# Optimization experiments

Measured on AMD Instinct MI355X. Metric: run time of the kernel, lower is better.

Reference implementation:

```python
import jax, jax.numpy as jnp
import numpy as np
import math

B, S, D, H, HD, M, E = 4, 1024, 1024, 16, 64, 4096, 1024
EPS = 1e-6

def rms_norm(x, w):
    # torch: x / (||x||/sqrt(d) + eps) * w  (eps added to the norm, not norm^2)
    n = jnp.sqrt(jnp.sum(x * x, axis=-1, keepdims=True)) / math.sqrt(x.shape[-1])
    return x / (n + EPS) * w

def rope(x):
    # x: (B,H,S,hd)
    hd, s = x.shape[-1], x.shape[2]
    inv = 1.0 / (10000.0 ** (jnp.arange(0, hd, 2, dtype=jnp.float32) / hd))
    fr = jnp.arange(s, dtype=jnp.float32)[:, None] * inv[None, :]        # (S, hd/2)
    emb = jnp.concatenate([fr, fr], axis=-1)                              # (S, hd)
    cos, sin = jnp.cos(emb), jnp.sin(emb)
    x1, x2 = x[..., : hd // 2], x[..., hd // 2 :]
    rot = jnp.concatenate([-x2, x1], axis=-1)
    return x * cos + rot * sin

def setup_inputs() -> dict:
    key = jax.random.key(0)
    ks = jax.random.split(key, 18)
    p = lambda k, sh: jax.random.normal(k, sh, jnp.float32) * 0.02
    return {
        'x': jax.random.normal(ks[0], (B, S, D), jnp.float32),
        'emb': jax.random.normal(ks[1], (B, E), jnp.float32),
        'ln1_w': jnp.ones((D,), jnp.float32),
        'ln1_lW': p(ks[2], (E, 2 * D)), 'ln1_lb': p(ks[3], (2 * D,)),
        'ln2_w': jnp.ones((D,), jnp.float32),
        'ln2_lW': p(ks[4], (E, 2 * D)), 'ln2_lb': p(ks[5], (2 * D,)),
        'qkv_W': p(ks[6], (D, 3 * D)), 'qkv_b': p(ks[7], (3 * D,)),
        'proj_W': p(ks[8], (D, D)), 'proj_b': p(ks[9], (D,)),
        'nq_w': jnp.ones((HD,), jnp.float32), 'nk_w': jnp.ones((HD,), jnp.float32),
        'mlp_W': p(ks[10], (D, 2 * M)), 'mlp_b': p(ks[11], (2 * M,)),
        'out_W': p(ks[12], (M, D)), 'out_b': p(ks[13], (D,)),
        'gates_W': p(ks[14], (E, 2 * D)), 'gates_b': p(ks[15], (2 * D,)),
    }

def reference(x, emb, ln1_w, ln1_lW, ln1_lb, ln2_w, ln2_lW, ln2_lb,
              qkv_W, qkv_b, proj_W, proj_b, nq_w, nk_w,
              mlp_W, mlp_b, out_W, out_b, gates_W, gates_b):
    g = emb @ gates_W + gates_b                       # (B, 2D)
    gate_mha, gate_mlp = g[:, :D], g[:, D:]
    # AdaLNZero 1
    ss = emb @ ln1_lW + ln1_lb                        # (B, 2D): [scale | shift]
    xn = rms_norm(x, ln1_w) * (1.0 + ss[:, None, :D]) + ss[:, None, D:]
    # RoPE attention with qk RMSNorm
    qkv = (xn @ qkv_W + qkv_b).reshape(B, S, 3, H, HD).transpose(2, 0, 3, 1, 4)
    q, k, v = qkv[0], qkv[1], qkv[2]                  # each (B,H,S,HD)
    q = rms_norm(rope(q), nq_w)
    k = rms_norm(rope(k), nk_w)
    scores = jnp.einsum('bhqd,bhkd->bhqk', q, k) * (HD ** -0.5)
    attn = jnp.nan_to_num(jax.nn.softmax(scores, axis=-1))
    ao = jnp.einsum('bhqk,bhkd->bhqd', attn, v).transpose(0, 2, 1, 3).reshape(B, S, D)
    x = x + gate_mha[:, None, :] * (ao @ proj_W + proj_b)
    # AdaLNZero 2 + SwiGLU MLP
    ss2 = emb @ ln2_lW + ln2_lb
    xn2 = rms_norm(x, ln2_w) * (1.0 + ss2[:, None, :D]) + ss2[:, None, D:]
    h = xn2 @ mlp_W + mlp_b                           # (B,S,2M)
    act = h[..., :M] * jax.nn.silu(h[..., M:])
    mlp_out = act @ out_W + out_b
    return x + gate_mlp[:, None, :] * mlp_out
```

## Files before the change

kernel.cpp:

```cpp
#include <hip/hip_runtime.h>
#include <hip/hip_bf16.h>
#include <math.h>

#define B_ 4
#define S_ 1024
#define D_ 1024
#define H_ 16
#define HD_ 64
#define M_ 4096
#define E_ 1024

using bf16 = __hip_bfloat16;
typedef short bf16x8 __attribute__((ext_vector_type(8)));
typedef float f32x4 __attribute__((ext_vector_type(4)));

__device__ __forceinline__ void gl_lds16(const void* g, void* l) {
    __builtin_amdgcn_global_load_lds(
        (__attribute__((address_space(1))) void*)(g),
        (__attribute__((address_space(3))) void*)(l), 16, 0, 0);
}



#define STG_A(q, pb, kc) gl_lds16(A  + gAoff[q] + (kc), &sA[pb][(q) * 4096 + tid * 8])
#define STG_B(q, pb, kc) gl_lds16(Bt + gBoff[q] + (kc), &sB[pb][(q) * 4096 + tid * 8])

#define LDA(mh, m, h) (*(const bf16x8*)(cA + aRow + (mh) * 8192 + (m) * 2048 + (h)))
#define LDB(nh, n, h) (*(const bf16x8*)(cB + bRow + (nh) * 4096 + (n) * 2048 + (h)))

#define MFMA_QUAD(MH, NH, BF)                                                             \
    __builtin_amdgcn_s_setprio(1);                                                        \
    _Pragma("unroll")                                                                     \
    for (int m = 0; m < 4; ++m) {                                                         \
        _Pragma("unroll")                                                                 \
        for (int n = 0; n < 2; ++n) {                                                     \
            acc[(MH)*4+m][(NH)*2+n] = __builtin_amdgcn_mfma_f32_16x16x32_bf16(            \
                aF[m][0], BF[n][0], acc[(MH)*4+m][(NH)*2+n], 0, 0, 0);                    \
            acc[(MH)*4+m][(NH)*2+n] = __builtin_amdgcn_mfma_f32_16x16x32_bf16(            \
                aF[m][1], BF[n][1], acc[(MH)*4+m][(NH)*2+n], 0, 0, 0);                    \
        }                                                                                 \
    }                                                                                     \
    __builtin_amdgcn_s_setprio(0);

#define GEMM256_LOOP                                                                      \
    const int nt = K >> 6;                                                                \
    for (int t = 0; t < nt; ++t) {                                                        \
        const int pb = t & 1;                                                             \
        const char* cA = (const char*)sA[pb];                                             \
        const char* cB = (const char*)sB[pb];                                             \
        const int kc2 = (t + 2) << 6;                                                     \
        const bool pf = (t + 2) < nt;                                                     \
        bf16x8 aF[4][2], b0F[2][2], b1F[2][2];                                            \
                                          \
        _Pragma("unroll")                                                                 \
        for (int m = 0; m < 4; ++m) {                                                     \
            aF[m][0] = LDA(0, m, cs0);                                                    \
            aF[m][1] = LDA(0, m, cs1);                                                    \
        }                                                                                 \
        _Pragma("unroll")                                                                 \
        for (int n = 0; n < 2; ++n) {                                                     \
            b0F[n][0] = LDB(0, n, cs0);                                                   \
            b0F[n][1] = LDB(0, n, cs1);                                                   \
        }                                                                                 \
        __builtin_amdgcn_s_barrier();                                                     \
        asm volatile("s_waitcnt lgkmcnt(0)" ::: "memory");                                \
        MFMA_QUAD(0, 0, b0F)                                                              \
        __builtin_amdgcn_s_barrier();                                                     \
                         \
        _Pragma("unroll")                                                                 \
        for (int n = 0; n < 2; ++n) {                                                     \
            b1F[n][0] = LDB(1, n, cs0);                                                   \
            b1F[n][1] = LDB(1, n, cs1);                                                   \
        }                                                                                 \
        if (pf) { STG_A(0, pb, kc2); STG_A(2, pb, kc2); }                                 \
        __builtin_amdgcn_s_barrier();                                                     \
        asm volatile("s_waitcnt lgkmcnt(0)" ::: "memory");                                \
        MFMA_QUAD(0, 1, b1F)                                                              \
        __builtin_amdgcn_s_barrier();                                                     \
                               \
        _Pragma("unroll")                                                                 \
        for (int m = 0; m < 4; ++m) {                                                     \
            aF[m][0] = LDA(1, m, cs0);                                                    \
            aF[m][1] = LDA(1, m, cs1);                                                    \
        }                                                                                 \
        if (pf) { STG_B(0, pb, kc2); STG_B(1, pb, kc2);                                   \
                  STG_B(2, pb, kc2); STG_B(3, pb, kc2); }                                 \
        __builtin_amdgcn_s_barrier();                                                     \
        asm volatile("s_waitcnt lgkmcnt(0)" ::: "memory");                                \
        MFMA_QUAD(1, 1, b1F)                                                              \
        __builtin_amdgcn_s_barrier();                                                     \
                                 \
        if (pf) { STG_A(1, pb, kc2); STG_A(3, pb, kc2); }                                 \
        __builtin_amdgcn_s_barrier();                                                     \
        asm volatile("s_waitcnt lgkmcnt(0)" ::: "memory");                                \
        MFMA_QUAD(1, 0, b0F)                                                              \
        if (pf)              { asm volatile("s_waitcnt vmcnt(8)" ::: "memory"); }         \
        else if (t + 1 < nt) { asm volatile("s_waitcnt vmcnt(0)" ::: "memory"); }         \
        __builtin_amdgcn_s_barrier();                                                     \
    }

#define GEMM256_PROLOG(NPN, N0MUL)                                                        \
    const int tid = threadIdx.x;                                                          \
    const int wave = tid >> 6, lane = tid & 63;                                           \
    const int wr = wave >> 2, wc = wave & 3;                                              \
    const int cl = lane & 15, qd = lane >> 4;                                             \
    const int num_pid_n = (NPN);                                                          \
    const int cpx = gridDim.x >> 3;                                                       \
    int wg = (blockIdx.x & 7) * cpx + (blockIdx.x >> 3);                                  \
    const int group_size = 8 * num_pid_n;                                                 \
    const int group_id = wg / group_size;                                                 \
    const int pid_in = wg - group_id * group_size;                                        \
    const int m0 = (group_id * 8 + (pid_in & 7)) * 256;                                   \
    const int n0 = (pid_in >> 3) * (N0MUL);

__global__ __launch_bounds__(256) void ropetab_kernel(float4* __restrict__ tab)
{
    int idx = blockIdx.x * 256 + threadIdx.x;
    int s = idx >> 4, j = idx & 15;
    float inv0 = exp2f(-(float)j        * (13.287712379549449f / 32.f));
    float inv1 = exp2f(-(float)(16 + j) * (13.287712379549449f / 32.f));
    float sn0, c0, sn1, c1;
    sincosf((float)s * inv0, &sn0, &c0);
    sincosf((float)s * inv1, &sn1, &c1);
    tab[idx] = make_float4(c0, sn0, c1, sn1);
}

__global__ __launch_bounds__(256) void transpose_all_kernel(
    const float* __restrict__ W0, bf16* __restrict__ T0,
    const float* __restrict__ W1, bf16* __restrict__ T1,
    const float* __restrict__ W2, bf16* __restrict__ T2,
    const float* __restrict__ W3, bf16* __restrict__ T3)
{
    __shared__ float tile[32][33];
    int id = blockIdx.x;
    const float* W; bf16* T; int K, N, bx, by;
    if (id < 3072)       { W = W0; T = T0; K = 1024; N = 3072; bx = id % 96;  by = id / 96; }
    else if (id < 4096)  { id -= 3072;  W = W1; T = T1; K = 1024; N = 1024; bx = id & 31;  by = id >> 5; }
    else if (id < 12288) { id -= 4096;  W = W2; T = T2; K = 1024; N = 8192; bx = id & 255; by = id >> 8; }
    else                 { id -= 12288; W = W3; T = T3; K = 4096; N = 1024; bx = id & 31;  by = id >> 5; }
    int n0 = bx * 32, k0 = by * 32;
    int tx = threadIdx.x & 31, ty = threadIdx.x >> 5;
    #pragma unroll
    for (int r = ty; r < 32; r += 8)
        tile[r][tx] = W[(long)(k0 + r) * N + n0 + tx];
    __syncthreads();
    #pragma unroll
    for (int r = ty; r < 32; r += 8)
        T[(long)(n0 + r) * K + k0 + tx] = __float2bfloat16(tile[tx][r]);
}

__global__ __launch_bounds__(256) void embgemm_kernel(
    const float* __restrict__ emb,
    const float* __restrict__ W0, const float* __restrict__ b0,
    const float* __restrict__ W1, const float* __restrict__ b1,
    const float* __restrict__ W2, const float* __restrict__ b2,
    float* __restrict__ G, float* __restrict__ SS, float* __restrict__ SS2)
{
    __shared__ float se[256];
    int b = blockIdx.y;
    int k0 = blockIdx.z * 256;
    if (threadIdx.x < 256) se[threadIdx.x] = emb[b * 1024 + k0 + threadIdx.x];
    __syncthreads();
    int j = blockIdx.x * 256 + threadIdx.x;
    int which = j >> 11, col = j & 2047;
    const float* W  = which == 0 ? W0 : (which == 1 ? W1 : W2);
    const float* bb = which == 0 ? b0 : (which == 1 ? b1 : b2);
    float acc = (k0 == 0) ? bb[col] : 0.f;
    #pragma unroll 4
    for (int k = 0; k < 256; ++k) acc += se[k] * W[(long)(k0 + k) * 2048 + col];
    float* out = which == 0 ? G : (which == 1 ? SS : SS2);
    atomicAdd(&out[b * 2048 + col], acc);
}

__global__ __launch_bounds__(256) void rmsmod_kernel(
    const float* __restrict__ x, const float* __restrict__ w,
    const float* __restrict__ ss, bf16* __restrict__ out)
{
    int row = blockIdx.x;
    int b = row >> 10;
    const float* xr = x + (long)row * D_;
    float4 v = ((const float4*)xr)[threadIdx.x];
    float ssum = v.x * v.x + v.y * v.y + v.z * v.z + v.w * v.w;
    #pragma unroll
    for (int off = 32; off; off >>= 1) ssum += __shfl_xor(ssum, off);
    __shared__ float red[4];
    if ((threadIdx.x & 63) == 0) red[threadIdx.x >> 6] = ssum;
    __syncthreads();
    float tot = red[0] + red[1] + red[2] + red[3];
    float n = sqrtf(tot) * (1.f / 32.f);
    float inv = 1.f / (n + 1e-6f);
    int d0 = threadIdx.x * 4;
    const float* ssb = ss + b * 2048;
    bf16 t[4];
    t[0] = __float2bfloat16(v.x * inv * w[d0 + 0] * (1.f + ssb[d0 + 0]) + ssb[D_ + d0 + 0]);
    t[1] = __float2bfloat16(v.y * inv * w[d0 + 1] * (1.f + ssb[d0 + 1]) + ssb[D_ + d0 + 1]);
    t[2] = __float2bfloat16(v.z * inv * w[d0 + 2] * (1.f + ssb[d0 + 2]) + ssb[D_ + d0 + 2]);
    t[3] = __float2bfloat16(v.w * inv * w[d0 + 3] * (1.f + ssb[d0 + 3]) + ssb[D_ + d0 + 3]);
    *(uint2*)&out[(long)row * D_ + d0] = *(uint2*)t;
}

__global__ __launch_bounds__(512) void qkvgemm_kernel(
    const bf16* __restrict__ A, const bf16* __restrict__ Bt,
    const float* __restrict__ bias,
    const float* __restrict__ nq_w, const float* __restrict__ nk_w,
    const float4* __restrict__ ropetab,
    bf16* __restrict__ qh, bf16* __restrict__ kh, bf16* __restrict__ vt,
    int N, int K)
{
    __shared__ bf16 sA[2][16384];
    __shared__ bf16 sB[2][16384];
    GEMM256_PROLOG(N >> 8, 256)

    long gAoff[4], gBoff[4];
    #pragma unroll
    for (int q = 0; q < 4; ++q) {
        int c = tid + q * 512;
        int cs = c ^ ((c >> 3) & 7);
        int row = cs >> 3, col = (cs & 7) * 8;
        gAoff[q] = (long)(m0 + row) * K + col;
        gBoff[q] = (long)(n0 + row) * K + col;
    }

    #pragma unroll
    for (int q = 0; q < 4; ++q) { STG_A(q, 0, 0); STG_B(q, 0, 0); }
    #pragma unroll
    for (int q = 0; q < 4; ++q) { STG_A(q, 1, 64); STG_B(q, 1, 64); }

    f32x4 acc[8][4] = {};
    const int swz = (cl & 7) << 4;
    const int aRow = (wr * 128 + cl) * 128;
    const int bRow = (wc * 64 + cl) * 128;
    const int cs0 = (qd * 16) ^ swz;
    const int cs1 = (qd * 16 + 64) ^ swz;

    asm volatile("s_waitcnt vmcnt(8)" ::: "memory");
    __builtin_amdgcn_s_barrier();

    GEMM256_LOOP

    const int third = n0 >> 10;
    const int h = ((n0 & 1023) >> 6) + wc;
    const int b = m0 >> 10;
    const int s0 = (m0 & 1023) + wr * 128;
    const int colb = n0 + wc * 64;
    float bs0 = bias[colb + cl],      bs1 = bias[colb + 16 + cl];
    float bs2 = bias[colb + 32 + cl], bs3 = bias[colb + 48 + cl];

    if (third == 2) {
        #pragma unroll
        for (int n = 0; n < 4; ++n) {
            int d = n * 16 + cl;
            float bs = bias[colb + n * 16 + cl];
            long rowd = ((long)(b * 16 + h) * 64 + d) * 1024;
            #pragma unroll
            for (int m = 0; m < 8; ++m) {
                int sb = s0 + m * 16 + qd * 4;
                bf16 t4[4];
                #pragma unroll
                for (int i = 0; i < 4; ++i)
                    t4[i] = __float2bfloat16(acc[m][n][i] + bs);
                *(uint2*)&vt[rowd + sb] = *(uint2*)t4;
            }
        }
    } else {
        const float* w = (third == 0) ? nq_w : nk_w;
        bf16* dst = (third == 0) ? qh : kh;
        float w0 = w[cl], w1 = w[16 + cl], w2 = w[32 + cl], w3 = w[48 + cl];
        long hb = ((long)(b * 16 + h) * 1024) * 64;
        #pragma unroll
        for (int m = 0; m < 8; ++m) {
            #pragma unroll
            for (int i = 0; i < 4; ++i) {
                int s = s0 + m * 16 + qd * 4 + i;
                float v0 = acc[m][0][i] + bs0, v1 = acc[m][1][i] + bs1;
                float v2 = acc[m][2][i] + bs2, v3 = acc[m][3][i] + bs3;
                float4 cs = ropetab[s * 16 + cl];
                float r0 = v0 * cs.x - v2 * cs.y;
                float r1 = v1 * cs.z - v3 * cs.w;
                float r2 = v2 * cs.x + v0 * cs.y;
                float r3 = v3 * cs.z + v1 * cs.w;
                float ssq = r0 * r0 + r1 * r1 + r2 * r2 + r3 * r3;
                ssq += __shfl_xor(ssq, 1);
                ssq += __shfl_xor(ssq, 2);
                ssq += __shfl_xor(ssq, 4);
                ssq += __shfl_xor(ssq, 8);
                float innv = 1.f / (sqrtf(ssq) * 0.125f + 1e-6f);
                long ro = hb + (long)s * 64;
                dst[ro + cl]      = __float2bfloat16(r0 * innv * w0);
                dst[ro + 16 + cl] = __float2bfloat16(r1 * innv * w1);
                dst[ro + 32 + cl] = __float2bfloat16(r2 * innv * w2);
                dst[ro + 48 + cl] = __float2bfloat16(r3 * innv * w3);
            }
        }
    }
}

__global__ __launch_bounds__(512) void gemm256_mlp_kernel(
    const bf16* __restrict__ A, const bf16* __restrict__ Bt,
    const float* __restrict__ bias, bf16* __restrict__ ACT, int K)
{
    __shared__ bf16 sA[2][16384];
    __shared__ bf16 sB[2][16384];
    GEMM256_PROLOG(32, 128)

    long gAoff[4], gBoff[4];
    #pragma unroll
    for (int q = 0; q < 4; ++q) {
        int c = tid + q * 512;
        int cs = c ^ ((c >> 3) & 7);
        int row = cs >> 3, col = (cs & 7) * 8;
        gAoff[q] = (long)(m0 + row) * K + col;
        int pp = row >> 5, hf = (row >> 4) & 1, wi = row & 15;
        gBoff[q] = (long)(hf * 4096 + n0 + pp * 16 + wi) * K + col;
    }

    #pragma unroll
    for (int q = 0; q < 4; ++q) { STG_A(q, 0, 0); STG_B(q, 0, 0); }
    #pragma unroll
    for (int q = 0; q < 4; ++q) { STG_A(q, 1, 64); STG_B(q, 1, 64); }

    f32x4 acc[8][4] = {};
    const int swz = (cl & 7) << 4;
    const int aRow = (wr * 128 + cl) * 128;
    const int bRow = (wc * 64 + cl) * 128;
    const int cs0 = (qd * 16) ^ swz;
    const int cs1 = (qd * 16 + 64) ^ swz;

    asm volatile("s_waitcnt vmcnt(8)" ::: "memory");
    __builtin_amdgcn_s_barrier();

    GEMM256_LOOP

    #pragma unroll
    for (int m = 0; m < 8; ++m) {
        #pragma unroll
        for (int pr = 0; pr < 2; ++pr) {
            int col = n0 + wc * 32 + pr * 16 + cl;
            float bs1 = bias[col];
            float bs2 = bias[4096 + col];
            #pragma unroll
            for (int i = 0; i < 4; ++i) {
                int row = m0 + wr * 128 + m * 16 + qd * 4 + i;
                float h1 = acc[m][pr * 2 + 0][i] + bs1;
                float h2 = acc[m][pr * 2 + 1][i] + bs2;
                float sg = 1.f / (1.f + __expf(-h2));
                ACT[(long)row * 4096 + col] = __float2bfloat16(h1 * h2 * sg);
            }
        }
    }
}

#define MFMA_HQ(MH)                                                                       \
    __builtin_amdgcn_s_setprio(1);                                                        \
    _Pragma("unroll")                                                                     \
    for (int m = 0; m < 4; ++m) {                                                         \
        _Pragma("unroll")                                                                 \
        for (int n = 0; n < 2; ++n) {                                                     \
            acc[(MH)*4+m][n] = __builtin_amdgcn_mfma_f32_16x16x32_bf16(                   \
                aF[m][0], bF[n][0], acc[(MH)*4+m][n], 0, 0, 0);                           \
            acc[(MH)*4+m][n] = __builtin_amdgcn_mfma_f32_16x16x32_bf16(                   \
                aF[m][1], bF[n][1], acc[(MH)*4+m][n], 0, 0, 0);                           \
        }                                                                                 \
    }                                                                                     \
    __builtin_amdgcn_s_setprio(0);

__global__ __launch_bounds__(512) void gemm256x128_kernel(
    const bf16* __restrict__ A, const bf16* __restrict__ Bt,
    float* __restrict__ P0, float* __restrict__ P1, int N, int K)
{
    __shared__ bf16 sA[2][16384];
    __shared__ bf16 sB[2][8192];
    const int tid = threadIdx.x;
    const int wave = tid >> 6, lane = tid & 63;
    const int wr = wave >> 2, wc = wave & 3;
    const int cl = lane & 15, qd = lane >> 4;

    const int cpx = gridDim.x >> 3;
    int wg = (blockIdx.x & 7) * cpx + (blockIdx.x >> 3);
    const int split = wg >> 7;
    const int w2 = wg & 127;
    const int group_id = w2 >> 6;
    const int pid_in = w2 & 63;
    const int m0 = (group_id * 8 + (pid_in & 7)) * 256;
    const int n0 = (pid_in >> 3) * 128;
    const int Kh = K >> 1;
    A  += (long)split * Kh;
    Bt += (long)split * Kh;

    long gAoff[4], gBoff[2];
    #pragma unroll
    for (int q = 0; q < 4; ++q) {
        int c = tid + q * 512;
        int cs = c ^ ((c >> 3) & 7);
        int row = cs >> 3, col = (cs & 7) * 8;
        gAoff[q] = (long)(m0 + row) * K + col;
        if (q < 2) gBoff[q] = (long)(n0 + row) * K + col;
    }

    const int nt = Kh >> 6;
    STG_A(0, 0, 0); STG_A(2, 0, 0); STG_B(0, 0, 0); STG_B(1, 0, 0);
    STG_A(1, 0, 0); STG_A(3, 0, 0);
    if (nt > 1) { STG_A(0, 1, 64); STG_A(2, 1, 64); STG_B(0, 1, 64); STG_B(1, 1, 64); }

    f32x4 acc[8][2] = {};
    const int swz = (cl & 7) << 4;
    const int aRow = (wr * 128 + cl) * 128;
    const int bRow = (wc * 32 + cl) * 128;
    const int cs0 = (qd * 16) ^ swz;
    const int cs1 = (qd * 16 + 64) ^ swz;

    if (nt > 1) { asm volatile("s_waitcnt vmcnt(4)" ::: "memory"); }
    else        { asm volatile("s_waitcnt vmcnt(0)" ::: "memory"); }
    __builtin_amdgcn_s_barrier();

    for (int t = 0; t < nt; ++t) {
        const int pb = t & 1;
        const char* cA = (const char*)sA[pb];
        const char* cB = (const char*)sB[pb];
        bf16x8 aF[4][2], bF[2][2];
        #pragma unroll
        for (int m = 0; m < 4; ++m) {
            aF[m][0] = *(const bf16x8*)(cA + aRow + m * 2048 + cs0);
            aF[m][1] = *(const bf16x8*)(cA + aRow + m * 2048 + cs1);
        }
        #pragma unroll
        for (int n = 0; n < 2; ++n) {
            bF[n][0] = *(const bf16x8*)(cB + bRow + n * 2048 + cs0);
            bF[n][1] = *(const bf16x8*)(cB + bRow + n * 2048 + cs1);
        }
        if (t + 1 < nt) { STG_A(1, pb ^ 1, (t + 1) << 6); STG_A(3, pb ^ 1, (t + 1) << 6); }
        __builtin_amdgcn_s_barrier();
        asm volatile("s_waitcnt lgkmcnt(0)" ::: "memory");
        MFMA_HQ(0)
        __builtin_amdgcn_s_barrier();
        #pragma unroll
        for (int m = 0; m < 4; ++m) {
            aF[m][0] = *(const bf16x8*)(cA + aRow + 8192 + m * 2048 + cs0);
            aF[m][1] = *(const bf16x8*)(cA + aRow + 8192 + m * 2048 + cs1);
        }
        if (t + 2 < nt) { STG_A(0, pb, (t + 2) << 6); STG_A(2, pb, (t + 2) << 6);
                          STG_B(0, pb, (t + 2) << 6); STG_B(1, pb, (t + 2) << 6); }
        __builtin_amdgcn_s_barrier();
        asm volatile("s_waitcnt lgkmcnt(0)" ::: "memory");
        MFMA_HQ(1)
        if (t + 2 < nt)      { asm volatile("s_waitcnt vmcnt(4)" ::: "memory"); }
        else if (t + 1 < nt) { asm volatile("s_waitcnt vmcnt(0)" ::: "memory"); }
        __builtin_amdgcn_s_barrier();
    }

    float* P = split ? P1 : P0;
    #pragma unroll
    for (int m = 0; m < 8; ++m) {
        #pragma unroll
        for (int n = 0; n < 2; ++n) {
            int col = n0 + wc * 32 + n * 16 + cl;
            #pragma unroll
            for (int i = 0; i < 4; ++i) {
                int row = m0 + wr * 128 + m * 16 + qd * 4 + i;
                P[(long)row * N + col] = acc[m][n][i];
            }
        }
    }
}

__global__ __launch_bounds__(256) void fuseout_kernel(
    const float* __restrict__ p0, const float* __restrict__ p1,
    const float* __restrict__ bias, const float* __restrict__ resid,
    const float* __restrict__ gates, float* __restrict__ out)
{
    int idx = blockIdx.x * 256 + threadIdx.x;
    int row = idx >> 8;
    int b = row >> 10;
    int c4 = (idx & 255) * 4;
    float4 a = ((const float4*)p0)[idx];
    float4 c = ((const float4*)p1)[idx];
    float4 r = ((const float4*)resid)[idx];
    float4 bb = *(const float4*)&bias[c4];
    float4 gg = *(const float4*)&gates[b * 2048 + 1024 + c4];
    float4 o;
    o.x = r.x + gg.x * (a.x + c.x + bb.x);
    o.y = r.y + gg.y * (a.y + c.y + bb.y);
    o.z = r.z + gg.z * (a.z + c.z + bb.z);
    o.w = r.w + gg.w * (a.w + c.w + bb.w);
    ((float4*)out)[idx] = o;
}

__global__ __launch_bounds__(256) void gemm64_kernel(
    const bf16* __restrict__ A, const bf16* __restrict__ Bt,
    const float* __restrict__ bias,
    bf16* __restrict__ Cb, float* __restrict__ Cf,
    const float* __restrict__ resid, const float* __restrict__ gates, int gate_off,
    int Mrows, int N, int K, int mode)
{
    __shared__ bf16 sA[64 * 32];
    __shared__ bf16 sB[64 * 32];
    const int tid = threadIdx.x;
    const int wave = tid >> 6, lane = tid & 63;
    const int num_pid_n = N >> 6;
    const int pid = blockIdx.x;
    const int group_size = 8 * num_pid_n;
    const int group_id = pid / group_size;
    const int pid_in = pid - group_id * group_size;
    const int pid_m = group_id * 8 + (pid_in & 7);
    const int pid_n = pid_in >> 3;
    const int m0 = pid_m * 64, n0 = pid_n * 64;
    const int wm = (wave & 1) * 32, wn = (wave >> 1) * 32;
    const int cl = lane & 15, qd = lane >> 4;

    f32x4 acc[2][2] = {};

    const int c = tid;
    const int rr = c >> 2, ss = (c & 3) ^ ((c >> 3) & 3);
    const bf16* gA = A + (long)(m0 + rr) * K + ss * 8;
    const bf16* gB = Bt + (long)(n0 + rr) * K + ss * 8;
    bf16* lA = &sA[wave * 512];
    bf16* lB = &sB[wave * 512];

    const int q8s = (qd ^ ((cl >> 1) & 3)) * 8;

    for (int kc = 0; kc < K; kc += 32) {
        gl_lds16(gA + kc, lA);
        gl_lds16(gB + kc, lB);
        __syncthreads();
        bf16x8 af[2], bfr[2];
        #pragma unroll
        for (int t = 0; t < 2; ++t)
            af[t] = *(const bf16x8*)&sA[(wm + cl + t * 16) * 32 + q8s];
        #pragma unroll
        for (int u = 0; u < 2; ++u)
            bfr[u] = *(const bf16x8*)&sB[(wn + cl + u * 16) * 32 + q8s];
        #pragma unroll
        for (int t = 0; t < 2; ++t)
            #pragma unroll
            for (int u = 0; u < 2; ++u)
                acc[t][u] = __builtin_amdgcn_mfma_f32_16x16x32_bf16(af[t], bfr[u], acc[t][u], 0, 0, 0);
        __syncthreads();
    }

    #pragma unroll
    for (int t = 0; t < 2; ++t) {
        #pragma unroll
        for (int u = 0; u < 2; ++u) {
            int col = n0 + wn + u * 16 + cl;
            float bs = bias[col];
            #pragma unroll
            for (int i = 0; i < 4; ++i) {
                int row = m0 + wm + t * 16 + qd * 4 + i;
                float v = acc[t][u][i] + bs;
                if (mode == 0) {
                    Cb[(long)row * N + col] = __float2bfloat16(v);
                } else {
                    int b = row >> 10;
                    float g = gates[b * 2048 + gate_off + col];
                    Cf[(long)row * N + col] = resid[(long)row * N + col] + g * v;
                }
            }
        }
    }
}

__global__ __launch_bounds__(256) void attn_kernel(
    const bf16* __restrict__ qh, const bf16* __restrict__ kh, const bf16* __restrict__ vt,
    bf16* __restrict__ ao)
{
    const int bh = blockIdx.y;
    const int q0 = blockIdx.x * 64;
    const int tid = threadIdx.x, wave = tid >> 6, lane = tid & 63;
    const int cl = lane & 15, qd = lane >> 4;

    __shared__ bf16 sQ[64 * 64];
    __shared__ bf16 sK[64 * 64];
    __shared__ bf16 sV[64 * 64];
    __shared__ bf16 sP[4][16 * 64];

    const int r0 = tid >> 3;
    const int c0 = (tid & 7) ^ (r0 & 7);
    const int r1 = (tid + 256) >> 3;
    const int c1 = ((tid + 256) & 7) ^ (r1 & 7);

    {
        const bf16* Qg = qh + (long)bh * S_ * 64 + (long)q0 * 64;
        gl_lds16(Qg + r0 * 64 + c0 * 8, &sQ[(long)tid * 8]);
        gl_lds16(Qg + r1 * 64 + c1 * 8, &sQ[(long)(tid + 256) * 8]);
    }

    float l_i[4] = {0.f, 0.f, 0.f, 0.f};
    f32x4 o_acc[4] = {};

    const bf16* Kg = kh + (long)bh * S_ * 64;
    const bf16* Vg = vt + (long)bh * 64 * S_;

    const int swz = (cl & 7) << 4;
    const char* cQ = (const char*)sQ;
    const char* cK = (const char*)sK;
    const char* cV = (const char*)sV;
    char* cP = (char*)sP[wave];
    const int aqRow = (wave * 16 + cl) * 128;

    for (int kv0 = 0; kv0 < S_; kv0 += 64) {
        __syncthreads();
        {
            gl_lds16(Kg + (long)(kv0 + r0) * 64 + c0 * 8, &sK[(long)tid * 8]);
            gl_lds16(Kg + (long)(kv0 + r1) * 64 + c1 * 8, &sK[(long)(tid + 256) * 8]);
            gl_lds16(Vg + (long)r0 * S_ + kv0 + c0 * 8, &sV[(long)tid * 8]);
            gl_lds16(Vg + (long)r1 * S_ + kv0 + c1 * 8, &sV[(long)(tid + 256) * 8]);
        }
        __syncthreads();

        f32x4 sfr[4] = {};
        #pragma unroll
        for (int ks = 0; ks < 2; ++ks) {
            const int co = (ks * 64 + qd * 16) ^ swz;
            bf16x8 aq = *(const bf16x8*)(cQ + aqRow + co);
            #pragma unroll
            for (int u = 0; u < 4; ++u) {
                bf16x8 bk = *(const bf16x8*)(cK + (u * 16 + cl) * 128 + co);
                sfr[u] = __builtin_amdgcn_mfma_f32_16x16x32_bf16(aq, bk, sfr[u], 0, 0, 0);
            }
        }

        #pragma unroll
        for (int i = 0; i < 4; ++i) {
            int rowp = qd * 4 + i;
            char* pb = cP + rowp * 128;
            const int xorv = (rowp & 7) << 4;
            float sum = 0.f;
            #pragma unroll
            for (int u = 0; u < 4; ++u) {
                float p = __expf(sfr[u][i] * 0.125f - 8.f);
                sum += p;
                *(bf16*)(pb + ((u * 32 + cl * 2) ^ xorv)) = __float2bfloat16(p);
            }
            sum += __shfl_xor(sum, 1);
            sum += __shfl_xor(sum, 2);
            sum += __shfl_xor(sum, 4);
            sum += __shfl_xor(sum, 8);
            l_i[i] += sum;
        }

        #pragma unroll
        for (int ks = 0; ks < 2; ++ks) {
            const int co = (ks * 64 + qd * 16) ^ swz;
            bf16x8 ap = *(const bf16x8*)(cP + cl * 128 + co);
            #pragma unroll
            for (int u = 0; u < 4; ++u) {
                bf16x8 bv = *(const bf16x8*)(cV + (u * 16 + cl) * 128 + co);
                o_acc[u] = __builtin_amdgcn_mfma_f32_16x16x32_bf16(ap, bv, o_acc[u], 0, 0, 0);
            }
        }
    }

    #pragma unroll
    for (int i = 0; i < 4; ++i) {
        float invl = 1.f / l_i[i];
        int row = q0 + wave * 16 + qd * 4 + i;
        #pragma unroll
        for (int u = 0; u < 4; ++u) {
            int d = u * 16 + cl;
            ao[((long)(bh >> 4) * S_ + row) * D_ + (bh & 15) * 64 + d] =
                __float2bfloat16(o_acc[u][i] * invl);
        }
    }
}

extern "C" void kernel_launch(void* const* d_in, const int* in_sizes, int n_in,
                              void* d_out, int out_size, void* d_ws, size_t ws_size,
                              hipStream_t stream) {
    const float* x       = (const float*)d_in[0];
    const float* emb     = (const float*)d_in[1];
    const float* ln1_w   = (const float*)d_in[2];
    const float* ln1_lW  = (const float*)d_in[3];
    const float* ln1_lb  = (const float*)d_in[4];
    const float* ln2_w   = (const float*)d_in[5];
    const float* ln2_lW  = (const float*)d_in[6];
    const float* ln2_lb  = (const float*)d_in[7];
    const float* qkv_W   = (const float*)d_in[8];
    const float* qkv_b   = (const float*)d_in[9];
    const float* proj_W  = (const float*)d_in[10];
    const float* proj_b  = (const float*)d_in[11];
    const float* nq_w    = (const float*)d_in[12];
    const float* nk_w    = (const float*)d_in[13];
    const float* mlp_W   = (const float*)d_in[14];
    const float* mlp_b   = (const float*)d_in[15];
    const float* out_W   = (const float*)d_in[16];
    const float* out_b   = (const float*)d_in[17];
    const float* gates_W = (const float*)d_in[18];
    const float* gates_b = (const float*)d_in[19];
    float* out = (float*)d_out;

    char* p = (char*)d_ws;
    if (ws_size < 159481856UL) return;
    bf16* WT_QKV  = (bf16*)p;  p += 6291456;
    bf16* WT_PROJ = (bf16*)p;  p += 2097152;
    bf16* WT_MLP  = (bf16*)p;  p += 16777216;
    bf16* WT_OUT  = (bf16*)p;  p += 8388608;
    float* G      = (float*)p; p += 32768;
    float* SSb    = (float*)p; p += 32768;
    float* SS2b   = (float*)p; p += 32768;
    float* X1     = (float*)p; p += 16777216;
    bf16* XN2     = (bf16*)p;  p += 8388608;
    bf16* ACT     = (bf16*)p;  p += 33554432;
    char* REG = p;
    bf16* XN   = (bf16*)(REG);
    bf16* QH   = (bf16*)(REG + 33554432);
    bf16* KH   = (bf16*)(REG + 41943040);
    bf16* VT   = (bf16*)(REG + 50331648);
    bf16* AO   = (bf16*)(REG + 58720256);
    float* PF0 = (float*)(REG);
    float* PF1 = (float*)(REG + 16777216);
    float4* ROPETAB = (float4*)X1;

    dim3 blk(256);
    hipMemsetAsync(G, 0, 98304, stream);
    ropetab_kernel<<<dim3(64), blk, 0, stream>>>(ROPETAB);
    transpose_all_kernel<<<dim3(16384), blk, 0, stream>>>(qkv_W, WT_QKV, proj_W, WT_PROJ,
                                                          mlp_W, WT_MLP, out_W, WT_OUT);
    embgemm_kernel<<<dim3(24, 4, 4), blk, 0, stream>>>(emb, gates_W, gates_b, ln1_lW, ln1_lb,
                                                       ln2_lW, ln2_lb, G, SSb, SS2b);
    rmsmod_kernel<<<dim3(4096), blk, 0, stream>>>(x, ln1_w, SSb, XN);
    qkvgemm_kernel<<<dim3(192), dim3(512), 0, stream>>>(XN, WT_QKV, qkv_b, nq_w, nk_w,
                                                        ROPETAB, QH, KH, VT, 3072, 1024);
    attn_kernel<<<dim3(16, 64), blk, 0, stream>>>(QH, KH, VT, AO);
    gemm64_kernel<<<dim3(1024), blk, 0, stream>>>(AO, WT_PROJ, proj_b, nullptr, X1,
                                                  x, G, 0, 4096, 1024, 1024, 1);
    rmsmod_kernel<<<dim3(4096), blk, 0, stream>>>(X1, ln2_w, SS2b, XN2);
    gemm256_mlp_kernel<<<dim3(512), dim3(512), 0, stream>>>(XN2, WT_MLP, mlp_b, ACT, 1024);
    gemm256x128_kernel<<<dim3(256), dim3(512), 0, stream>>>(ACT, WT_OUT, PF0, PF1, 1024, 4096);
    fuseout_kernel<<<dim3(4096), blk, 0, stream>>>(PF0, PF1, out_b, X1, G, out);
}
```

Measured before the change: 451.8 us.

## Merge prep kernels into one launch and double-buffer K/V loads in attention

Folds the RoPE table, weight transpose and embedding GEMM kernels into a single block-indexed prep kernel, removing two launches and their gaps. Double-buffers the K/V LDS tiles in the attention kernel so the next tile is prefetched with global_load_lds while the current one is computed, using vmcnt waits and raw barriers. This doubles K/V LDS use, which may reduce occupancy, and relies on correct vmcnt accounting.

```diff
diff --git a/kernel.cpp b/kernel.cpp
--- a/kernel.cpp
+++ b/kernel.cpp
@@ -113,58 +113,58 @@
     const int m0 = (group_id * 8 + (pid_in & 7)) * 256;                                   \
     const int n0 = (pid_in >> 3) * (N0MUL);
 
-__global__ __launch_bounds__(256) void ropetab_kernel(float4* __restrict__ tab)
-{
-    int idx = blockIdx.x * 256 + threadIdx.x;
-    int s = idx >> 4, j = idx & 15;
-    float inv0 = exp2f(-(float)j        * (13.287712379549449f / 32.f));
-    float inv1 = exp2f(-(float)(16 + j) * (13.287712379549449f / 32.f));
-    float sn0, c0, sn1, c1;
-    sincosf((float)s * inv0, &sn0, &c0);
-    sincosf((float)s * inv1, &sn1, &c1);
-    tab[idx] = make_float4(c0, sn0, c1, sn1);
-}
-
-__global__ __launch_bounds__(256) void transpose_all_kernel(
+__global__ __launch_bounds__(256) void prep_kernel(
+    float4* __restrict__ tab,
     const float* __restrict__ W0, bf16* __restrict__ T0,
     const float* __restrict__ W1, bf16* __restrict__ T1,
     const float* __restrict__ W2, bf16* __restrict__ T2,
-    const float* __restrict__ W3, bf16* __restrict__ T3)
+    const float* __restrict__ W3, bf16* __restrict__ T3,
+    const float* __restrict__ emb,
+    const float* __restrict__ gW, const float* __restrict__ gb,
+    const float* __restrict__ l1W, const float* __restrict__ l1b,
+    const float* __restrict__ l2W, const float* __restrict__ l2b,
+    float* __restrict__ G, float* __restrict__ SS, float* __restrict__ SS2)
 {
     __shared__ float tile[32][33];
+    __shared__ float se[256];
     int id = blockIdx.x;
-    const float* W; bf16* T; int K, N, bx, by;
-    if (id < 3072)       { W = W0; T = T0; K = 1024; N = 3072; bx = id % 96;  by = id / 96; }
-    else if (id < 4096)  { id -= 3072;  W = W1; T = T1; K = 1024; N = 1024; bx = id & 31;  by = id >> 5; }
-    else if (id < 12288) { id -= 4096;  W = W2; T = T2; K = 1024; N = 8192; bx = id & 255; by = id >> 8; }
-    else                 { id -= 12288; W = W3; T = T3; K = 4096; N = 1024; bx = id & 31;  by = id >> 5; }
-    int n0 = bx * 32, k0 = by * 32;
-    int tx = threadIdx.x & 31, ty = threadIdx.x >> 5;
-    #pragma unroll
-    for (int r = ty; r < 32; r += 8)
-        tile[r][tx] = W[(long)(k0 + r) * N + n0 + tx];
-    __syncthreads();
-    #pragma unroll
-    for (int r = ty; r < 32; r += 8)
-        T[(long)(n0 + r) * K + k0 + tx] = __float2bfloat16(tile[tx][r]);
-}
-
-__global__ __launch_bounds__(256) void embgemm_kernel(
-    const float* __restrict__ emb,
-    const float* __restrict__ W0, const float* __restrict__ b0,
-    const float* __restrict__ W1, const float* __restrict__ b1,
-    const float* __restrict__ W2, const float* __restrict__ b2,
-    float* __restrict__ G, float* __restrict__ SS, float* __restrict__ SS2)
-{
-    __shared__ float se[256];
-    int b = blockIdx.y;
-    int k0 = blockIdx.z * 256;
+    if (id < 64) {
+        int idx = id * 256 + threadIdx.x;
+        int s = idx >> 4, j = idx & 15;
+        float inv0 = exp2f(-(float)j        * (13.287712379549449f / 32.f));
+        float inv1 = exp2f(-(float)(16 + j) * (13.287712379549449f / 32.f));
+        float sn0, c0, sn1, c1;
+        sincosf((float)s * inv0, &sn0, &c0);
+        sincosf((float)s * inv1, &sn1, &c1);
+        tab[idx] = make_float4(c0, sn0, c1, sn1);
+        return;
+    }
+    if (id < 16448) {
+        id -= 64;
+        const float* W; bf16* T; int K, N, bx, by;
+        if (id < 3072)       { W = W0; T = T0; K = 1024; N = 3072; bx = id % 96;  by = id / 96; }
+        else if (id < 4096)  { id -= 3072;  W = W1; T = T1; K = 1024; N = 1024; bx = id & 31;  by = id >> 5; }
+        else if (id < 12288) { id -= 4096;  W = W2; T = T2; K = 1024; N = 8192; bx = id & 255; by = id >> 8; }
+        else                 { id -= 12288; W = W3; T = T3; K = 4096; N = 1024; bx = id & 31;  by = id >> 5; }
+        int n0 = bx * 32, k0 = by * 32;
+        int tx = threadIdx.x & 31, ty = threadIdx.x >> 5;
+        #pragma unroll
+        for (int r = ty; r < 32; r += 8)
+            tile[r][tx] = W[(long)(k0 + r) * N + n0 + tx];
+        __syncthreads();
+        #pragma unroll
+        for (int r = ty; r < 32; r += 8)
+            T[(long)(n0 + r) * K + k0 + tx] = __float2bfloat16(tile[tx][r]);
+        return;
+    }
+    id -= 16448;
+    int bx = id % 24, b = (id / 24) & 3, k0 = (id / 96) * 256;
     if (threadIdx.x < 256) se[threadIdx.x] = emb[b * 1024 + k0 + threadIdx.x];
     __syncthreads();
-    int j = blockIdx.x * 256 + threadIdx.x;
+    int j = bx * 256 + threadIdx.x;
     int which = j >> 11, col = j & 2047;
-    const float* W  = which == 0 ? W0 : (which == 1 ? W1 : W2);
-    const float* bb = which == 0 ? b0 : (which == 1 ? b1 : b2);
+    const float* W  = which == 0 ? gW : (which == 1 ? l1W : l2W);
+    const float* bb = which == 0 ? gb : (which == 1 ? l1b : l2b);
     float acc = (k0 == 0) ? bb[col] : 0.f;
     #pragma unroll 4
     for (int k = 0; k < 256; ++k) acc += se[k] * W[(long)(k0 + k) * 2048 + col];
@@ -569,8 +569,8 @@
     const int cl = lane & 15, qd = lane >> 4;
 
     __shared__ bf16 sQ[64 * 64];
-    __shared__ bf16 sK[64 * 64];
-    __shared__ bf16 sV[64 * 64];
+    __shared__ bf16 sK[2][64 * 64];
+    __shared__ bf16 sV[2][64 * 64];
     __shared__ bf16 sP[4][16 * 64];
 
     const int r0 = tid >> 3;
@@ -578,34 +578,42 @@
     const int r1 = (tid + 256) >> 3;
     const int c1 = ((tid + 256) & 7) ^ (r1 & 7);
 
+    const bf16* Kg = kh + (long)bh * S_ * 64;
+    const bf16* Vg = vt + (long)bh * 64 * S_;
+
+    #define ATTN_STAGE(t) {                                                          \
+        int kv = (t) * 64;                                                           \
+        gl_lds16(Kg + (long)(kv + r0) * 64 + c0 * 8, &sK[(t) & 1][(long)tid * 8]);   \
+        gl_lds16(Kg + (long)(kv + r1) * 64 + c1 * 8, &sK[(t) & 1][(long)(tid + 256) * 8]); \
+        gl_lds16(Vg + (long)r0 * S_ + kv + c0 * 8, &sV[(t) & 1][(long)tid * 8]);     \
+        gl_lds16(Vg + (long)r1 * S_ + kv + c1 * 8, &sV[(t) & 1][(long)(tid + 256) * 8]); }
+
     {
         const bf16* Qg = qh + (long)bh * S_ * 64 + (long)q0 * 64;
         gl_lds16(Qg + r0 * 64 + c0 * 8, &sQ[(long)tid * 8]);
         gl_lds16(Qg + r1 * 64 + c1 * 8, &sQ[(long)(tid + 256) * 8]);
+        ATTN_STAGE(0)
     }
 
     float l_i[4] = {0.f, 0.f, 0.f, 0.f};
     f32x4 o_acc[4] = {};
 
-    const bf16* Kg = kh + (long)bh * S_ * 64;
-    const bf16* Vg = vt + (long)bh * 64 * S_;
-
     const int swz = (cl & 7) << 4;
     const char* cQ = (const char*)sQ;
-    const char* cK = (const char*)sK;
-    const char* cV = (const char*)sV;
     char* cP = (char*)sP[wave];
     const int aqRow = (wave * 16 + cl) * 128;
 
-    for (int kv0 = 0; kv0 < S_; kv0 += 64) {
-        __syncthreads();
-        {
-            gl_lds16(Kg + (long)(kv0 + r0) * 64 + c0 * 8, &sK[(long)tid * 8]);
-            gl_lds16(Kg + (long)(kv0 + r1) * 64 + c1 * 8, &sK[(long)(tid + 256) * 8]);
-            gl_lds16(Vg + (long)r0 * S_ + kv0 + c0 * 8, &sV[(long)tid * 8]);
-            gl_lds16(Vg + (long)r1 * S_ + kv0 + c1 * 8, &sV[(long)(tid + 256) * 8]);
-        }
-        __syncthreads();
+    for (int t = 0; t < 16; ++t) {
+        __builtin_amdgcn_s_barrier();
+        if (t + 1 < 16) {
+            ATTN_STAGE(t + 1)
+            asm volatile("s_waitcnt vmcnt(4)" ::: "memory");
+        } else {
+            asm volatile("s_waitcnt vmcnt(0)" ::: "memory");
+        }
+        __builtin_amdgcn_s_barrier();
+        const char* cK = (const char*)sK[t & 1];
+        const char* cV = (const char*)sV[t & 1];
 
         f32x4 sfr[4] = {};
         #pragma unroll
@@ -649,6 +657,7 @@
             }
         }
     }
+    #undef ATTN_STAGE
 
     #pragma unroll
     for (int i = 0; i < 4; ++i) {
@@ -712,11 +721,11 @@
 
     dim3 blk(256);
     hipMemsetAsync(G, 0, 98304, stream);
-    ropetab_kernel<<<dim3(64), blk, 0, stream>>>(ROPETAB);
-    transpose_all_kernel<<<dim3(16384), blk, 0, stream>>>(qkv_W, WT_QKV, proj_W, WT_PROJ,
-                                                          mlp_W, WT_MLP, out_W, WT_OUT);
-    embgemm_kernel<<<dim3(24, 4, 4), blk, 0, stream>>>(emb, gates_W, gates_b, ln1_lW, ln1_lb,
-                                                       ln2_lW, ln2_lb, G, SSb, SS2b);
+    prep_kernel<<<dim3(16832), blk, 0, stream>>>(ROPETAB,
+                                                 qkv_W, WT_QKV, proj_W, WT_PROJ,
+                                                 mlp_W, WT_MLP, out_W, WT_OUT,
+                                                 emb, gates_W, gates_b, ln1_lW, ln1_lb,
+                                                 ln2_lW, ln2_lb, G, SSb, SS2b);
     rmsmod_kernel<<<dim3(4096), blk, 0, stream>>>(x, ln1_w, SSb, XN);
     qkvgemm_kernel<<<dim3(192), dim3(512), 0, stream>>>(XN, WT_QKV, qkv_b, nq_w, nk_w,
                                                         ROPETAB, QH, KH, VT, 3072, 1024);
```

Result: no change. 452.9 us (+0.2%).
